# Kernel tuning notes

Hardware: AMD Instinct MI355X
Metric: run time of the kernel (lower is better)

Reference implementation:

```python
import jax, jax.numpy as jnp
import numpy as np

IN_C = 128
MID_C = 128
EPS = 1e-5


def layer_norm(x, g, b):
    mu = jnp.mean(x, axis=-1, keepdims=True)
    var = jnp.mean(jnp.square(x - mu), axis=-1, keepdims=True)
    return (x - mu) * jax.lax.rsqrt(var + EPS) * g + b


def setup_inputs() -> dict:
    key = jax.random.key(0)
    ks = jax.random.split(key, 16)
    B, N = 1, 384
    s_in = 1.0 / np.sqrt(IN_C)
    s_mid = 1.0 / np.sqrt(MID_C)
    return {
        "x2d": jax.random.normal(ks[0], (B, N, N, IN_C), dtype=jnp.float32),
        "n1_g": jnp.ones((IN_C,), jnp.float32),
        "n1_b": jnp.zeros((IN_C,), jnp.float32),
        "n2_g": jnp.ones((MID_C,), jnp.float32),
        "n2_b": jnp.zeros((MID_C,), jnp.float32),
        "w1i": jax.random.uniform(ks[1], (MID_C, IN_C), jnp.float32, -s_in, s_in),
        "b1i": jnp.zeros((MID_C,), jnp.float32),
        "w1j": jax.random.uniform(ks[2], (MID_C, IN_C), jnp.float32, -s_in, s_in),
        "b1j": jnp.zeros((MID_C,), jnp.float32),
        "w1i_s": jax.random.uniform(ks[3], (MID_C, IN_C), jnp.float32, -s_in, s_in),
        "b1i_s": jnp.zeros((MID_C,), jnp.float32),
        "w1j_s": jax.random.uniform(ks[4], (MID_C, IN_C), jnp.float32, -s_in, s_in),
        "b1j_s": jnp.zeros((MID_C,), jnp.float32),
        "w2": jax.random.uniform(ks[5], (IN_C, MID_C), jnp.float32, -s_mid, s_mid),
        "b2": jnp.zeros((IN_C,), jnp.float32),
        "w3": jax.random.uniform(ks[6], (IN_C, IN_C), jnp.float32, -s_in, s_in),
        "b3": jnp.zeros((IN_C,), jnp.float32),
    }


def reference(x2d, n1_g, n1_b, n2_g, n2_b, w1i, b1i, w1j, b1j,
              w1i_s, b1i_s, w1j_s, b1j_s, w2, b2, w3, b3):
    # x2d: [B, N, N, C]
    x = layer_norm(x2d, n1_g, n1_b)
    i = (x @ w1i.T + b1i) * jax.nn.sigmoid(x @ w1i_s.T + b1i_s)  # [B,N,N,mid]
    j = (x @ w1j.T + b1j) * jax.nn.sigmoid(x @ w1j_s.T + b1j_s)  # [B,N,N,mid]
    out = jnp.einsum('bikc,bjkc->bijc', i, j)                    # contract over k
    out = layer_norm(out, n2_g, n2_b)
    out = out @ w2.T + b2
    out = out * jax.nn.sigmoid(x @ w3.T + b3)
    return out
```

## Files before the change

kernel.cpp:

```cpp
#include <hip/hip_runtime.h>

#define NN 384
#define CC 128
#define NPOS (NN * NN)

typedef short bf8_t __attribute__((ext_vector_type(8)));
typedef float f32x4_t __attribute__((ext_vector_type(4)));

#define MFMA16(a, b, c) __builtin_amdgcn_mfma_f32_16x16x32_bf16((a), (b), (c), 0, 0, 0)

__device__ __forceinline__ unsigned short f2bf(float f) {
  unsigned int u = __builtin_bit_cast(unsigned int, f);
  u += 0x7fffu + ((u >> 16) & 1u);
  return (unsigned short)(u >> 16);
}
__device__ __forceinline__ float bf2f(unsigned short s) {
  return __builtin_bit_cast(float, ((unsigned int)s) << 16);
}
__device__ __forceinline__ float sigm(float x) { return 1.0f / (1.0f + __expf(-x)); }

__global__ __launch_bounds__(256) void kW(const float* __restrict__ a,
                                          const float* __restrict__ b,
                                          const float* __restrict__ c,
                                          const float* __restrict__ d,
                                          const float* __restrict__ e,
                                          const float* __restrict__ f,
                                          unsigned short* __restrict__ o) {
  int idx = (blockIdx.x * 256 + threadIdx.x) * 4;
  const float* s = f;
  if (idx < 16384) s = a;
  else if (idx < 32768) s = b;
  else if (idx < 49152) s = c;
  else if (idx < 65536) s = d;
  else if (idx < 81920) s = e;
  int off = idx & 16383;
  float4 v = *(const float4*)(s + off);
  o[idx + 0] = f2bf(v.x);
  o[idx + 1] = f2bf(v.y);
  o[idx + 2] = f2bf(v.z);
  o[idx + 3] = f2bf(v.w);
}

__global__ __launch_bounds__(256) void kLN(const float* __restrict__ x,
                                           const float* __restrict__ n1g,
                                           const float* __restrict__ n1b,
                                           unsigned short* __restrict__ x_ln) {
  int t = threadIdx.x;
  int pos = blockIdx.x * 128 + (t >> 1);
  int half = t & 1;
  const float* xr = x + (size_t)pos * CC + half * 64;
  float v[64];
  float s = 0.f;
#pragma unroll
  for (int a = 0; a < 16; ++a) {
    float4 f4 = ((const float4*)xr)[a];
    v[4 * a + 0] = f4.x; v[4 * a + 1] = f4.y;
    v[4 * a + 2] = f4.z; v[4 * a + 3] = f4.w;
    s += f4.x + f4.y + f4.z + f4.w;
  }
  s += __shfl_xor(s, 1);
  float mu = s * (1.0f / CC);
  float vs = 0.f;
#pragma unroll
  for (int a = 0; a < 64; ++a) { float d = v[a] - mu; vs += d * d; }
  vs += __shfl_xor(vs, 1);
  float rs = rsqrtf(vs * (1.0f / CC) + 1e-5f);
  unsigned short* dst = x_ln + (size_t)pos * CC + half * 64;
#pragma unroll
  for (int a8 = 0; a8 < 8; ++a8) {
    union { bf8_t v8; unsigned short e[8]; } u;
#pragma unroll
    for (int e = 0; e < 8; ++e) {
      int c = half * 64 + a8 * 8 + e;
      u.e[e] = f2bf((v[a8 * 8 + e] - mu) * rs * n1g[c] + n1b[c]);
    }
    *(bf8_t*)(dst + a8 * 8) = u.v8;
  }
}

__global__ __launch_bounds__(256, 2) void kP(
    const unsigned short* __restrict__ x_ln, const unsigned short* __restrict__ wcat,
    const float* __restrict__ b1i, const float* __restrict__ b1is,
    const float* __restrict__ b1j, const float* __restrict__ b1js,
    const float* __restrict__ b3v, unsigned short* __restrict__ i_s,
    unsigned short* __restrict__ j_s, unsigned short* __restrict__ g3) {
  __shared__ __align__(16) unsigned short lds[16640];
  float* bl = (float*)(lds + 16384);

  int b = blockIdx.x;
  int pt = b / 6, job = b % 6;
  int p = job >> 1, h = job & 1;
  int p0 = pt * 128;
  int t = threadIdx.x, lane = t & 63, wave = t >> 6;
  int lr = lane & 15, lh = lane >> 4;

  bf8_t xf[2][4];
#pragma unroll
  for (int nt = 0; nt < 2; ++nt)
#pragma unroll
    for (int kk = 0; kk < 4; ++kk)
      xf[nt][kk] = *(const bf8_t*)(x_ln + (size_t)(p0 + wave * 32 + nt * 16 + lr) * CC +
                                   kk * 32 + lh * 8);

  int mV = p * 2;
  const unsigned short* Wv = wcat + (size_t)mV * CC * CC + h * 64 * CC;
#pragma unroll
  for (int it = 0; it < 4; ++it) {
    int u = it * 256 + t;
    int row = u >> 4, sl = u & 15;
    int slg = sl ^ (row & 7);
    __builtin_amdgcn_global_load_lds(
        (const __attribute__((address_space(1))) unsigned int*)(Wv + row * CC + slg * 8),
        (__attribute__((address_space(3))) unsigned int*)(lds + u * 8), 16, 0, 0);
  }
  if (p < 2) {
    const unsigned short* Wg = wcat + (size_t)(mV + 1) * CC * CC + h * 64 * CC;
#pragma unroll
    for (int it = 0; it < 4; ++it) {
      int u = it * 256 + t;
      int row = u >> 4, sl = u & 15;
      int slg = sl ^ (row & 7);
      __builtin_amdgcn_global_load_lds(
          (const __attribute__((address_space(1))) unsigned int*)(Wg + row * CC + slg * 8),
          (__attribute__((address_space(3))) unsigned int*)(lds + 8192 + u * 8), 16, 0, 0);
    }
  }
  {
    const float* bvp = (p == 0) ? b1i : (p == 1) ? b1j : b3v;
    if (t < 16) ((float4*)bl)[t] = ((const float4*)(bvp + h * 64))[t];
    if (p < 2 && t >= 16 && t < 32) {
      const float* bgp = (p == 0) ? b1is : b1js;
      ((float4*)bl)[t] = ((const float4*)(bgp + h * 64))[t - 16];
    }
  }
  __syncthreads();

  f32x4_t z4 = {0.f, 0.f, 0.f, 0.f};
  f32x4_t accV[2][4], accG[2][4];
#pragma unroll
  for (int nt = 0; nt < 2; ++nt)
#pragma unroll
    for (int ct = 0; ct < 4; ++ct) { accV[nt][ct] = z4; accG[nt][ct] = z4; }
#pragma unroll
  for (int ct = 0; ct < 4; ++ct)
#pragma unroll
    for (int kk = 0; kk < 4; ++kk) {
      int rv = ct * 16 + lr;
      int slot = (kk * 4 + lh) ^ (rv & 7);
      bf8_t wv = *(const bf8_t*)&lds[rv * 128 + slot * 8];
      if (p < 2) {
        bf8_t wg = *(const bf8_t*)&lds[8192 + rv * 128 + slot * 8];
#pragma unroll
        for (int nt = 0; nt < 2; ++nt) {
          accV[nt][ct] = MFMA16(wv, xf[nt][kk], accV[nt][ct]);
          accG[nt][ct] = MFMA16(wg, xf[nt][kk], accG[nt][ct]);
        }
      } else {
#pragma unroll
        for (int nt = 0; nt < 2; ++nt)
          accV[nt][ct] = MFMA16(xf[nt][kk], wv, accV[nt][ct]);
      }
    }
  __syncthreads();

  if (p < 2) {
#pragma unroll
    for (int nt = 0; nt < 2; ++nt)
#pragma unroll
      for (int ct = 0; ct < 4; ++ct)
#pragma unroll
        for (int r = 0; r < 4; ++r) {
          int cl = ct * 16 + lh * 4 + r;
          int pos = wave * 32 + nt * 16 + lr;
          float o = (accV[nt][ct][r] + bl[cl]) * sigm(accG[nt][ct][r] + bl[64 + cl]);
          int sw = ((ct * 4 + lh) & 7) << 4;
          lds[cl * 128 + (pos ^ sw)] = f2bf(o);
        }
    __syncthreads();
    unsigned short* dstm = p ? j_s : i_s;
#pragma unroll
    for (int it = 0; it < 4; ++it) {
      int u = it * 256 + t;
      int cl = u >> 4, ch = u & 15;
      int s = (cl >> 2) & 7;
      bf8_t v = *(const bf8_t*)&lds[cl * 128 + ((ch ^ (s << 1)) * 8)];
      *(bf8_t*)(dstm + (size_t)(h * 64 + cl) * NPOS + p0 + ch * 8) = v;
    }
  } else {
#pragma unroll
    for (int nt = 0; nt < 2; ++nt)
#pragma unroll
      for (int ct = 0; ct < 4; ++ct)
#pragma unroll
        for (int r = 0; r < 4; ++r) {
          int pos = wave * 32 + nt * 16 + lh * 4 + r;
          int cl = ct * 16 + lr;
          float o = sigm(accV[nt][ct][r] + bl[cl]);
          int slot = (cl >> 3) ^ (pos & 7);
          lds[pos * 64 + slot * 8 + (cl & 7)] = f2bf(o);
        }
    __syncthreads();
#pragma unroll
    for (int it = 0; it < 4; ++it) {
      int u = it * 256 + t;
      int pos = u >> 3, ch = u & 7;
      int slot = ch ^ (pos & 7);
      bf8_t v = *(const bf8_t*)&lds[pos * 64 + slot * 8];
      *(bf8_t*)(g3 + (size_t)(p0 + pos) * CC + h * 64 + ch * 8) = v;
    }
  }
}

__global__ __launch_bounds__(256) void kB(const unsigned short* __restrict__ i_s,
                                          const unsigned short* __restrict__ j_s,
                                          float* __restrict__ out_pre) {
  __shared__ unsigned short At[128][32];
  __shared__ unsigned short Bt[128][32];
  int b = blockIdx.x;
  int logical = (b & 7) * 144 + (b >> 3);
  int c = logical / 9;
  int tt = logical % 9;
  int i0 = (tt / 3) * 128, j0 = (tt % 3) * 128;
  const unsigned short* Ab = i_s + ((size_t)c * NN + i0) * NN;
  const unsigned short* Bb = j_s + ((size_t)c * NN + j0) * NN;
  int t = threadIdx.x, lane = t & 63, wave = t >> 6;
  int wi = (wave >> 1) * 64, wj = (wave & 1) * 64;
  int lr = lane & 15, lh = lane >> 4;
  int rsub = lane >> 2;
  int ksub = (lane & 3) * 8;

  f32x4_t z4 = {0.f, 0.f, 0.f, 0.f};
  f32x4_t acc[4][4];
#pragma unroll
  for (int mt = 0; mt < 4; ++mt)
#pragma unroll
    for (int nt = 0; nt < 4; ++nt) acc[mt][nt] = z4;

  for (int k0 = 0; k0 < NN; k0 += 32) {
#pragma unroll
    for (int half = 0; half < 2; ++half) {
      int r = half * 64 + wave * 16;
      __builtin_amdgcn_global_load_lds(
          (const __attribute__((address_space(1))) unsigned int*)(Ab + (size_t)(r + rsub) * NN + k0 + ksub),
          (__attribute__((address_space(3))) unsigned int*)&At[r][0], 16, 0, 0);
      __builtin_amdgcn_global_load_lds(
          (const __attribute__((address_space(1))) unsigned int*)(Bb + (size_t)(r + rsub) * NN + k0 + ksub),
          (__attribute__((address_space(3))) unsigned int*)&Bt[r][0], 16, 0, 0);
    }
    __syncthreads();
    bf8_t af2[4], bf2[4];
#pragma unroll
    for (int mt = 0; mt < 4; ++mt) af2[mt] = *(const bf8_t*)&At[wi + mt * 16 + lr][lh * 8];
#pragma unroll
    for (int nt = 0; nt < 4; ++nt) bf2[nt] = *(const bf8_t*)&Bt[wj + nt * 16 + lr][lh * 8];
#pragma unroll
    for (int mt = 0; mt < 4; ++mt)
#pragma unroll
      for (int nt = 0; nt < 4; ++nt) acc[mt][nt] = MFMA16(af2[mt], bf2[nt], acc[mt][nt]);
    __syncthreads();
  }
  float* orow = out_pre + ((size_t)c * NN + (i0 + wi)) * NN + (j0 + wj);
#pragma unroll
  for (int mt = 0; mt < 4; ++mt)
#pragma unroll
    for (int nt = 0; nt < 4; ++nt)
#pragma unroll
      for (int r = 0; r < 4; ++r)
        orow[(size_t)(mt * 16 + lh * 4 + r) * NN + nt * 16 + lr] = acc[mt][nt][r];
}

__global__ __launch_bounds__(256) void kC(const float* __restrict__ out_pre,
                                          const float* __restrict__ n2g,
                                          const float* __restrict__ n2b,
                                          const unsigned short* __restrict__ w2bf,
                                          const float* __restrict__ b2,
                                          const unsigned short* __restrict__ g3,
                                          float* __restrict__ out) {
  __shared__ unsigned short xs2[128][136];
  int b = blockIdx.x;
  int ii = b / 3, j0 = (b % 3) * 128;
  int t = threadIdx.x, lane = t & 63, wave = t >> 6;
  {
    int pos = t >> 1, half = t & 1;
    const float* src = out_pre + (size_t)half * 64 * NPOS + (size_t)ii * NN + j0 + pos;
    float v[64];
    float s = 0.f;
#pragma unroll
    for (int a2 = 0; a2 < 64; ++a2) { v[a2] = src[(size_t)a2 * NPOS]; s += v[a2]; }
    s += __shfl_xor(s, 1);
    float mu = s * (1.0f / CC);
    float vs = 0.f;
#pragma unroll
    for (int a2 = 0; a2 < 64; ++a2) { float d = v[a2] - mu; vs += d * d; }
    vs += __shfl_xor(vs, 1);
    float rs = rsqrtf(vs * (1.0f / CC) + 1e-5f);
#pragma unroll
    for (int a8 = 0; a8 < 8; ++a8) {
      union { bf8_t v8; unsigned short e[8]; } u;
#pragma unroll
      for (int e2 = 0; e2 < 8; ++e2) {
        int c = half * 64 + a8 * 8 + e2;
        u.e[e2] = f2bf((v[a8 * 8 + e2] - mu) * rs * n2g[c] + n2b[c]);
      }
      *(bf8_t*)&xs2[pos][half * 64 + a8 * 8] = u.v8;
    }
  }
  __syncthreads();
  int lr = lane & 15, lh = lane >> 4;
  bf8_t af2[2][4];
#pragma unroll
  for (int mt = 0; mt < 2; ++mt)
#pragma unroll
    for (int kk = 0; kk < 4; ++kk)
      af2[mt][kk] = *(const bf8_t*)&xs2[wave * 32 + mt * 16 + lr][kk * 32 + lh * 8];
  f32x4_t z4 = {0.f, 0.f, 0.f, 0.f};
  f32x4_t acc[2][8];
#pragma unroll
  for (int mt = 0; mt < 2; ++mt)
#pragma unroll
    for (int nt = 0; nt < 8; ++nt) acc[mt][nt] = z4;
#pragma unroll
  for (int nt = 0; nt < 8; ++nt) {
#pragma unroll
    for (int kk = 0; kk < 4; ++kk) {
      bf8_t bw = *(const bf8_t*)(w2bf + (size_t)(nt * 16 + lr) * CC + kk * 32 + lh * 8);
#pragma unroll
      for (int mt = 0; mt < 2; ++mt) acc[mt][nt] = MFMA16(af2[mt][kk], bw, acc[mt][nt]);
    }
  }
#pragma unroll
  for (int mt = 0; mt < 2; ++mt)
#pragma unroll
    for (int nt = 0; nt < 8; ++nt)
#pragma unroll
      for (int r = 0; r < 4; ++r) {
        int posl = wave * 32 + mt * 16 + lh * 4 + r;
        int c = nt * 16 + lr;
        size_t p = (size_t)ii * NN + j0 + posl;
        float y = acc[mt][nt][r] + b2[c];
        out[p * CC + c] = y * bf2f(g3[p * CC + c]);
      }
}

extern "C" void kernel_launch(void* const* d_in, const int* in_sizes, int n_in,
                              void* d_out, int out_size, void* d_ws, size_t ws_size,
                              hipStream_t stream) {
  (void)in_sizes; (void)n_in; (void)out_size; (void)ws_size;
  const float* x2d  = (const float*)d_in[0];
  const float* n1g  = (const float*)d_in[1];
  const float* n1b  = (const float*)d_in[2];
  const float* n2g  = (const float*)d_in[3];
  const float* n2b  = (const float*)d_in[4];
  const float* w1i  = (const float*)d_in[5];
  const float* b1i  = (const float*)d_in[6];
  const float* w1j  = (const float*)d_in[7];
  const float* b1j  = (const float*)d_in[8];
  const float* w1is = (const float*)d_in[9];
  const float* b1is = (const float*)d_in[10];
  const float* w1js = (const float*)d_in[11];
  const float* b1js = (const float*)d_in[12];
  const float* w2   = (const float*)d_in[13];
  const float* b2   = (const float*)d_in[14];
  const float* w3   = (const float*)d_in[15];
  const float* b3   = (const float*)d_in[16];

  char* ws = (char*)d_ws;
  unsigned short* wcat = (unsigned short*)ws;
  size_t TELEMS = (size_t)CC * NN * NN;
  unsigned short* i_s  = (unsigned short*)(ws + 262144);
  unsigned short* j_s  = i_s + TELEMS;
  unsigned short* g3   = j_s + TELEMS;
  unsigned short* x_ln = g3 + TELEMS;
  float* out_pre = (float*)x_ln;
  float* outp = (float*)d_out;

  kW<<<96, 256, 0, stream>>>(w1i, w1is, w1j, w1js, w3, w2, wcat);
  kLN<<<1152, 256, 0, stream>>>(x2d, n1g, n1b, x_ln);
  kP<<<6912, 256, 0, stream>>>(x_ln, wcat, b1i, b1is, b1j, b1js, b3, i_s, j_s, g3);
  kB<<<1152, 256, 0, stream>>>(i_s, j_s, out_pre);
  kC<<<1152, 256, 0, stream>>>(out_pre, n2g, n2b, wcat + 5 * CC * CC, b2, g3, outp);
}
```

Baseline: 195.0 us.

## Stage out_pre via async LDS loads in kC, remap kP blocks per XCD, hoist biases

In kC, the strided per-channel global reads of out_pre are replaced by coalesced global_load_lds transfers of a 128-channel by 128-position tile into a 64KB LDS buffer. The layer norm then reads from LDS, and the launch bound asks for 2 blocks per CU. The goal is to remove uncoalesced global reads with large strides, at the cost of more LDS use per block and an extra barrier. kP also remaps block indices so consecutive tiles land on the same XCD for L2 locality, and hoists bias values from LDS into registers before the epilogue.

Measured after the change: 195.8 us. No clear change (+0.4%).

```diff
diff --git a/kernel.cpp b/kernel.cpp
--- a/kernel.cpp
+++ b/kernel.cpp
@@ -88,7 +88,9 @@
   float* bl = (float*)(lds + 16384);
 
   int b = blockIdx.x;
-  int pt = b / 6, job = b % 6;
+  int xcd = b & 7, m = b >> 3;
+  int tl = m / 6, job = m % 6;
+  int pt = xcd * 144 + tl;
   int p = job >> 1, h = job & 1;
   int p0 = pt * 128;
   int t = threadIdx.x, lane = t & 63, wave = t >> 6;
@@ -135,6 +137,20 @@
   }
   __syncthreads();
 
+  float blv[16], blg[16];
+  if (p < 2) {
+#pragma unroll
+    for (int ct = 0; ct < 4; ++ct)
+#pragma unroll
+      for (int r = 0; r < 4; ++r) {
+        blv[ct * 4 + r] = bl[ct * 16 + lh * 4 + r];
+        blg[ct * 4 + r] = bl[64 + ct * 16 + lh * 4 + r];
+      }
+  } else {
+#pragma unroll
+    for (int ct = 0; ct < 4; ++ct) blv[ct] = bl[ct * 16 + lr];
+  }
+
   f32x4_t z4 = {0.f, 0.f, 0.f, 0.f};
   f32x4_t accV[2][4], accG[2][4];
 #pragma unroll
@@ -172,7 +188,8 @@
         for (int r = 0; r < 4; ++r) {
           int cl = ct * 16 + lh * 4 + r;
           int pos = wave * 32 + nt * 16 + lr;
-          float o = (accV[nt][ct][r] + bl[cl]) * sigm(accG[nt][ct][r] + bl[64 + cl]);
+          float o = (accV[nt][ct][r] + blv[ct * 4 + r]) *
+                    sigm(accG[nt][ct][r] + blg[ct * 4 + r]);
           int sw = ((ct * 4 + lh) & 7) << 4;
           lds[cl * 128 + (pos ^ sw)] = f2bf(o);
         }
@@ -195,7 +212,7 @@
         for (int r = 0; r < 4; ++r) {
           int pos = wave * 32 + nt * 16 + lh * 4 + r;
           int cl = ct * 16 + lr;
-          float o = sigm(accV[nt][ct][r] + bl[cl]);
+          float o = sigm(accV[nt][ct][r] + blv[ct]);
           int slot = (cl >> 3) ^ (pos & 7);
           lds[pos * 64 + slot * 8 + (cl & 7)] = f2bf(o);
         }
@@ -269,50 +286,62 @@
         orow[(size_t)(mt * 16 + lh * 4 + r) * NN + nt * 16 + lr] = acc[mt][nt][r];
 }
 
-__global__ __launch_bounds__(256) void kC(const float* __restrict__ out_pre,
-                                          const float* __restrict__ n2g,
-                                          const float* __restrict__ n2b,
-                                          const unsigned short* __restrict__ w2bf,
-                                          const float* __restrict__ b2,
-                                          const unsigned short* __restrict__ g3,
-                                          float* __restrict__ out) {
-  __shared__ unsigned short xs2[128][136];
+__global__ __launch_bounds__(256, 2) void kC(const float* __restrict__ out_pre,
+                                             const float* __restrict__ n2g,
+                                             const float* __restrict__ n2b,
+                                             const unsigned short* __restrict__ w2bf,
+                                             const float* __restrict__ b2,
+                                             const unsigned short* __restrict__ g3,
+                                             float* __restrict__ out) {
+  __shared__ __align__(16) float ldsf[16384];
+  unsigned short* xs2 = (unsigned short*)ldsf;
   int b = blockIdx.x;
   int ii = b / 3, j0 = (b % 3) * 128;
   int t = threadIdx.x, lane = t & 63, wave = t >> 6;
+
+#pragma unroll
+  for (int it = 0; it < 16; ++it) {
+    int u = it * 256 + t;
+    int c = u >> 5, jg = u & 31;
+    __builtin_amdgcn_global_load_lds(
+        (const __attribute__((address_space(1))) unsigned int*)(out_pre + ((size_t)c * NN + ii) * NN + j0 + jg * 4),
+        (__attribute__((address_space(3))) unsigned int*)(ldsf + u * 4), 16, 0, 0);
+  }
+  __syncthreads();
+
   {
     int pos = t >> 1, half = t & 1;
-    const float* src = out_pre + (size_t)half * 64 * NPOS + (size_t)ii * NN + j0 + pos;
     float v[64];
     float s = 0.f;
 #pragma unroll
-    for (int a2 = 0; a2 < 64; ++a2) { v[a2] = src[(size_t)a2 * NPOS]; s += v[a2]; }
+    for (int a = 0; a < 64; ++a) { v[a] = ldsf[(half * 64 + a) * 128 + pos]; s += v[a]; }
     s += __shfl_xor(s, 1);
     float mu = s * (1.0f / CC);
     float vs = 0.f;
 #pragma unroll
-    for (int a2 = 0; a2 < 64; ++a2) { float d = v[a2] - mu; vs += d * d; }
+    for (int a = 0; a < 64; ++a) { float d = v[a] - mu; vs += d * d; }
     vs += __shfl_xor(vs, 1);
     float rs = rsqrtf(vs * (1.0f / CC) + 1e-5f);
-#pragma unroll
-    for (int a8 = 0; a8 < 8; ++a8) {
-      union { bf8_t v8; unsigned short e[8]; } u;
-#pragma unroll
-      for (int e2 = 0; e2 < 8; ++e2) {
-        int c = half * 64 + a8 * 8 + e2;
-        u.e[e2] = f2bf((v[a8 * 8 + e2] - mu) * rs * n2g[c] + n2b[c]);
-      }
-      *(bf8_t*)&xs2[pos][half * 64 + a8 * 8] = u.v8;
-    }
+    union { bf8_t v8[8]; unsigned short e[64]; } u;
+#pragma unroll
+    for (int a = 0; a < 64; ++a) {
+      int c = half * 64 + a;
+      u.e[a] = f2bf((v[a] - mu) * rs * n2g[c] + n2b[c]);
+    }
+    __syncthreads();
+#pragma unroll
+    for (int a8 = 0; a8 < 8; ++a8)
+      *(bf8_t*)&xs2[pos * 136 + half * 64 + a8 * 8] = u.v8[a8];
   }
   __syncthreads();
+
   int lr = lane & 15, lh = lane >> 4;
   bf8_t af2[2][4];
 #pragma unroll
   for (int mt = 0; mt < 2; ++mt)
 #pragma unroll
     for (int kk = 0; kk < 4; ++kk)
-      af2[mt][kk] = *(const bf8_t*)&xs2[wave * 32 + mt * 16 + lr][kk * 32 + lh * 8];
+      af2[mt][kk] = *(const bf8_t*)&xs2[(wave * 32 + mt * 16 + lr) * 136 + kk * 32 + lh * 8];
   f32x4_t z4 = {0.f, 0.f, 0.f, 0.f};
   f32x4_t acc[2][8];
 #pragma unroll
```
